# Optimization experiments

Hardware: AMD Instinct MI355X
Metric: run time of the kernel (lower is better)

The kernel has to match this reference:

```python
import jax, jax.numpy as jnp
import numpy as np

H = 512

def _gru_layer(x, W_ih, W_hh, b_ih, b_hh):
    # x: [T, B, D_in]; PyTorch gate order: r, z, n
    xg = jnp.einsum('tbd,gd->tbg', x, W_ih) + b_ih  # [T, B, 3H], input projections for all steps
    h0 = jnp.zeros((x.shape[1], W_hh.shape[1]), x.dtype)

    def step(h, xg_t):
        hg = h @ W_hh.T + b_hh                      # [B, 3H]
        xr, xz, xn = jnp.split(xg_t, 3, axis=-1)
        hr, hz, hn = jnp.split(hg, 3, axis=-1)
        r = jax.nn.sigmoid(xr + hr)
        z = jax.nn.sigmoid(xz + hz)
        n = jnp.tanh(xn + r * hn)
        h_new = (1.0 - z) * n + z * h
        return h_new, h_new

    hT, ys = jax.lax.scan(step, h0, xg)
    return ys, hT  # [T, B, H], [B, H]


def setup_inputs() -> dict:
    key = jax.random.key(0)
    ks = jax.random.split(key, 10)
    D, T, B, L = 256, 512, 64, 2
    s = 1.0 / np.sqrt(H)  # PyTorch uniform(-1/sqrt(H), 1/sqrt(H)) init
    u = lambda k, shape: jax.random.uniform(k, shape, jnp.float32, -s, s)
    return {
        'x': jax.random.normal(ks[0], (T, B, D), jnp.float32),
        'W_ih0': u(ks[1], (3 * H, D)),
        'W_hh0': u(ks[2], (3 * H, H)),
        'b_ih0': u(ks[3], (3 * H,)),
        'b_hh0': u(ks[4], (3 * H,)),
        'W_ih1': u(ks[5], (3 * H, H)),
        'W_hh1': u(ks[6], (3 * H, H)),
        'b_ih1': u(ks[7], (3 * H,)),
        'b_hh1': u(ks[8], (3 * H,)),
    }


def reference(x, W_ih0, W_hh0, b_ih0, b_hh0, W_ih1, W_hh1, b_ih1, b_hh1):
    y0, h0 = _gru_layer(x, W_ih0, W_hh0, b_ih0, b_hh0)
    y1, h1 = _gru_layer(y0, W_ih1, W_hh1, b_ih1, b_hh1)
    hn = jnp.stack([h0, h1], axis=0)  # [num_layers, B, H]
    return (y1, hn)
```

## Files before the change

kernel.cpp:

```cpp
#include <hip/hip_runtime.h>
#include <math.h>

#define Hh   512
#define G3   1536
#define Tlen 512
#define Bsz  64
#define BH   (Bsz*Hh)

__device__ __forceinline__ float sigmoid_f(float x) { return 1.0f / (1.0f + expf(-x)); }

__device__ __forceinline__ void store_coh(float* p, float v) {
  asm volatile("global_store_dword %0, %1, off sc0 sc1" :: "v"(p), "v"(v) : "memory");
}

__global__ __launch_bounds__(256) void gemm_xg(const float* __restrict__ A,
                                               const float* __restrict__ W,
                                               const float* __restrict__ bias,
                                               float* __restrict__ C,
                                               int M, int N, int K) {
  __shared__ float As[16][132];
  __shared__ float Bs[16][132];
  const int nbm = M >> 7;
  const int bm = blockIdx.x % nbm;
  const int bn = blockIdx.x / nbm;
  const int m0 = bm << 7, n0 = bn << 7;
  const int tid = threadIdx.x;
  const int tx = tid & 15, ty = tid >> 4;

  const int row0 = tid >> 2;
  const int kq0  = (tid & 3) << 2;

  const float* Ap0 = &A[(size_t)(m0 + row0) * K + kq0];
  const float* Ap1 = &A[(size_t)(m0 + row0 + 64) * K + kq0];
  const float* Wp0 = &W[(size_t)(n0 + row0) * K + kq0];
  const float* Wp1 = &W[(size_t)(n0 + row0 + 64) * K + kq0];

  float4 ra0 = *(const float4*)(Ap0);
  float4 ra1 = *(const float4*)(Ap1);
  float4 rb0 = *(const float4*)(Wp0);
  float4 rb1 = *(const float4*)(Wp1);

  float acc[8][8];
#pragma unroll
  for (int r = 0; r < 8; r++)
#pragma unroll
    for (int c = 0; c < 8; c++) acc[r][c] = 0.0f;

  for (int kk = 0; kk < K; kk += 16) {
    As[kq0+0][row0]    = ra0.x; As[kq0+1][row0]    = ra0.y; As[kq0+2][row0]    = ra0.z; As[kq0+3][row0]    = ra0.w;
    As[kq0+0][row0+64] = ra1.x; As[kq0+1][row0+64] = ra1.y; As[kq0+2][row0+64] = ra1.z; As[kq0+3][row0+64] = ra1.w;
    Bs[kq0+0][row0]    = rb0.x; Bs[kq0+1][row0]    = rb0.y; Bs[kq0+2][row0]    = rb0.z; Bs[kq0+3][row0]    = rb0.w;
    Bs[kq0+0][row0+64] = rb1.x; Bs[kq0+1][row0+64] = rb1.y; Bs[kq0+2][row0+64] = rb1.z; Bs[kq0+3][row0+64] = rb1.w;
    __syncthreads();
    const int kn = kk + 16;
    if (kn < K) {
      ra0 = *(const float4*)(Ap0 + kn);
      ra1 = *(const float4*)(Ap1 + kn);
      rb0 = *(const float4*)(Wp0 + kn);
      rb1 = *(const float4*)(Wp1 + kn);
    }
#pragma unroll
    for (int k = 0; k < 16; k++) {
      float4 a0 = *(const float4*)&As[k][ty << 3];
      float4 a1 = *(const float4*)&As[k][(ty << 3) + 4];
      float4 b0 = *(const float4*)&Bs[k][tx << 3];
      float4 b1 = *(const float4*)&Bs[k][(tx << 3) + 4];
      float ar[8] = {a0.x, a0.y, a0.z, a0.w, a1.x, a1.y, a1.z, a1.w};
      float br[8] = {b0.x, b0.y, b0.z, b0.w, b1.x, b1.y, b1.z, b1.w};
#pragma unroll
      for (int r = 0; r < 8; r++)
#pragma unroll
        for (int c = 0; c < 8; c++) acc[r][c] = fmaf(ar[r], br[c], acc[r][c]);
    }
    __syncthreads();
  }
  float bl[8];
#pragma unroll
  for (int c = 0; c < 8; c++) bl[c] = bias[n0 + (tx << 3) + c];
#pragma unroll
  for (int r = 0; r < 8; r++) {
    int m = m0 + (ty << 3) + r;
    float4 o0 = make_float4(acc[r][0] + bl[0], acc[r][1] + bl[1], acc[r][2] + bl[2], acc[r][3] + bl[3]);
    float4 o1 = make_float4(acc[r][4] + bl[4], acc[r][5] + bl[5], acc[r][6] + bl[6], acc[r][7] + bl[7]);
    *(float4*)&C[(size_t)m * N + n0 + (tx << 3)]     = o0;
    *(float4*)&C[(size_t)m * N + n0 + (tx << 3) + 4] = o1;
  }
}

__global__ __launch_bounds__(256, 1) void gru_scan(
    const float* __restrict__ xg,
    const float* __restrict__ Whh,
    const float* __restrict__ bhh,
    float* __restrict__ y,
    float* __restrict__ hfin,
    float* hbuf,
    int* slots,
    int base) {
  const int tid = threadIdx.x;
  const int jl = tid >> 4;
  const int ks = tid & 15;
  const int bgrp = blockIdx.x & 7;
  const int jgrp = blockIdx.x >> 3;
  const int j0 = jgrp << 4;
  const int b0 = bgrp << 3;
  const int k0 = ks << 5;

  int* myslot = slots + (bgrp * 32 + jgrp) * 32;
  int* gslots = slots + bgrp * 32 * 32;

  __shared__ float4 hs4[8 * 128];

  float4 wv[3][8];
#pragma unroll
  for (int g = 0; g < 3; g++) {
    const float* wp = &Whh[(size_t)(g * Hh + j0 + jl) * Hh + k0];
#pragma unroll
    for (int q = 0; q < 8; q++) wv[g][q] = *(const float4*)&wp[q * 4];
  }
  float bh[3];
#pragma unroll
  for (int g = 0; g < 3; g++) bh[g] = bhh[g * Hh + j0 + jl];

  int off[8];
#pragma unroll
  for (int q = 0; q < 8; q++) off[q] = (ks * 8 + q) ^ (ks & 7);

  const int fq = tid & 127;
  const int brow = tid >> 7;
  const int fswz = fq ^ ((fq >> 3) & 7);

  float xr = 0.0f, xz = 0.0f, xn = 0.0f;
  if (ks < 8) {
    const float* xp = &xg[(size_t)(b0 + ks) * G3 + j0 + jl];
    xr = xp[0]; xz = xp[Hh]; xn = xp[2 * Hh];
  }

  int cur = 0;

  for (int t = 0; t < Tlen; t++) {
    const float4* hsrc = (const float4*)(hbuf + cur * BH) + (size_t)(b0 + brow) * 128 + fq;
    float4 h0, h1, h2, h3;
    {
      const float4* p0 = hsrc;
      const float4* p1 = hsrc + 2 * 128;
      const float4* p2 = hsrc + 4 * 128;
      const float4* p3 = hsrc + 6 * 128;
      asm volatile(
          "global_load_dwordx4 %0, %4, off sc0 sc1\n\t"
          "global_load_dwordx4 %1, %5, off sc0 sc1\n\t"
          "global_load_dwordx4 %2, %6, off sc0 sc1\n\t"
          "global_load_dwordx4 %3, %7, off sc0 sc1\n\t"
          "s_waitcnt vmcnt(0)"
          : "=&v"(h0), "=&v"(h1), "=&v"(h2), "=&v"(h3)
          : "v"(p0), "v"(p1), "v"(p2), "v"(p3)
          : "memory");
    }
    hs4[(brow + 0) * 128 + fswz] = h0;
    hs4[(brow + 2) * 128 + fswz] = h1;
    hs4[(brow + 4) * 128 + fswz] = h2;
    hs4[(brow + 6) * 128 + fswz] = h3;
    __syncthreads();

    float acc[3][8];
#pragma unroll
    for (int b = 0; b < 8; b++) {
      float4 hv[8];
#pragma unroll
      for (int q = 0; q < 8; q++) hv[q] = hs4[b * 128 + off[q]];
#pragma unroll
      for (int g = 0; g < 3; g++) {
        float s = 0.0f;
#pragma unroll
        for (int q = 0; q < 8; q++) {
          s = fmaf(wv[g][q].x, hv[q].x, s);
          s = fmaf(wv[g][q].y, hv[q].y, s);
          s = fmaf(wv[g][q].z, hv[q].z, s);
          s = fmaf(wv[g][q].w, hv[q].w, s);
        }
        acc[g][b] = s;
      }
    }
#pragma unroll
    for (int d = 1; d < 16; d <<= 1) {
#pragma unroll
      for (int g = 0; g < 3; g++)
#pragma unroll
        for (int b = 0; b < 8; b++) acc[g][b] += __shfl_xor(acc[g][b], d);
    }

    if (ks < 8) {
      int b = b0 + ks;
      int e = j0 + jl;
      float r = sigmoid_f(xr + acc[0][ks] + bh[0]);
      float z = sigmoid_f(xz + acc[1][ks] + bh[1]);
      float n = tanhf(xn + r * (acc[2][ks] + bh[2]));
      int f = e >> 2;
      float4 hp4 = hs4[ks * 128 + (f ^ ((f >> 3) & 7))];
      float hp = ((const float*)&hp4)[e & 3];
      float hnew = (1.0f - z) * n + z * hp;
      store_coh(&hbuf[(cur ^ 1) * BH + (size_t)b * Hh + e], hnew);
      y[((size_t)t * Bsz + b) * Hh + e] = hnew;
      if (t == Tlen - 1) hfin[(size_t)b * Hh + e] = hnew;
    }

    if (t == Tlen - 1) break;

    __syncthreads();

    if (tid == 0) {
      __hip_atomic_store(myslot, base + t + 1, __ATOMIC_RELAXED, __HIP_MEMORY_SCOPE_AGENT);
    }

    float nxr = 0.0f, nxz = 0.0f, nxn = 0.0f;
    if (ks < 8) {
      const float* xp = &xg[((size_t)(t + 1) * Bsz + (b0 + ks)) * G3 + j0 + jl];
      nxr = xp[0]; nxz = xp[Hh]; nxn = xp[2 * Hh];
    }

    if (tid < 64) {
      const int target = base + t + 1;
      for (;;) {
        int v = (tid < 32)
            ? __hip_atomic_load(gslots + tid * 32, __ATOMIC_RELAXED, __HIP_MEMORY_SCOPE_AGENT)
            : 0x7FFFFFFF;
        if (!__any(v < target)) break;
        __builtin_amdgcn_s_sleep(1);
      }
    }
    __syncthreads();

    xr = nxr; xz = nxz; xn = nxn;
    cur ^= 1;
  }
}

extern "C" void kernel_launch(void* const* d_in, const int* in_sizes, int n_in,
                              void* d_out, int out_size, void* d_ws, size_t ws_size,
                              hipStream_t stream) {
  const float* x     = (const float*)d_in[0];
  const float* Wih0  = (const float*)d_in[1];
  const float* Whh0  = (const float*)d_in[2];
  const float* bih0  = (const float*)d_in[3];
  const float* bhh0  = (const float*)d_in[4];
  const float* Wih1  = (const float*)d_in[5];
  const float* Whh1  = (const float*)d_in[6];
  const float* bih1  = (const float*)d_in[7];
  const float* bhh1  = (const float*)d_in[8];

  float* out = (float*)d_out;
  float* y1   = out;
  float* hn0  = out + (size_t)Tlen * BH;
  float* hn1  = hn0 + BH;

  float* ws    = (float*)d_ws;
  int*   slots = (int*)d_ws;
  float* hbuf  = ws + 8192;
  float* xgbuf = hbuf + 4 * BH;
  float* y0    = xgbuf + (size_t)Tlen * Bsz * G3;

  const int M = Tlen * Bsz;

  hipMemsetAsync(slots, 0, 8 * 32 * 32 * sizeof(int), stream);
  hipMemsetAsync(hbuf, 0, BH * sizeof(float), stream);
  hipMemsetAsync(hbuf + 2 * BH, 0, BH * sizeof(float), stream);

  dim3 gemm_grid((M / 128) * (G3 / 128));

  gemm_xg<<<gemm_grid, 256, 0, stream>>>(x, Wih0, bih0, xgbuf, M, G3, 256);
  gru_scan<<<256, 256, 0, stream>>>(xgbuf, Whh0, bhh0, y0, hn0, hbuf, slots, 0);

  gemm_xg<<<gemm_grid, 256, 0, stream>>>(y0, Wih1, bih1, xgbuf, M, G3, 512);
  gru_scan<<<256, 256, 0, stream>>>(xgbuf, Whh1, bhh1, y1, hn1, hbuf + 2 * BH, slots, Tlen);
}
```

Baseline: 5.867 ms.

## Fuse both GRU layers into one wavefront-pipelined persistent kernel

Replaces the two sequential scan kernels and the second input-projection GEMM with a single persistent kernel of 512 blocks. Half the blocks run layer 0 and the other half run layer 1, which computes its input projection per step from y0 using register-resident Wih1. Layer 1 waits on per-step flags from layer 0 and from its own blocks, so the two recurrences overlap in a wavefront instead of running back to back. The cost is double the register weight footprint for layer-1 blocks and a launch-bounds occupancy of 2 blocks per CU. It also adds cross-layer spin-wait traffic and relies on all 512 blocks being co-resident to avoid deadlock.

```diff
diff --git a/kernel.cpp b/kernel.cpp
--- a/kernel.cpp
+++ b/kernel.cpp
@@ -87,150 +87,304 @@
   }
 }
 
-__global__ __launch_bounds__(256, 1) void gru_scan(
-    const float* __restrict__ xg,
-    const float* __restrict__ Whh,
-    const float* __restrict__ bhh,
-    float* __restrict__ y,
-    float* __restrict__ hfin,
-    float* hbuf,
-    int* slots,
-    int base) {
+__global__ __launch_bounds__(256, 2) void gru_fused(
+    const float* __restrict__ xg0,
+    const float* __restrict__ Whh0,
+    const float* __restrict__ bhh0,
+    const float* __restrict__ Wih1,
+    const float* __restrict__ bih1,
+    const float* __restrict__ Whh1,
+    const float* __restrict__ bhh1,
+    float* __restrict__ y1,
+    float* __restrict__ hn0,
+    float* __restrict__ hn1,
+    float* h0buf, float* h1buf,
+    float* y0buf,
+    int* l0slots, int* l1slots) {
   const int tid = threadIdx.x;
   const int jl = tid >> 4;
   const int ks = tid & 15;
   const int bgrp = blockIdx.x & 7;
-  const int jgrp = blockIdx.x >> 3;
+  const int rr   = blockIdx.x >> 3;
+  const int role = rr & 1;
+  const int jgrp = rr >> 1;
   const int j0 = jgrp << 4;
   const int b0 = bgrp << 3;
   const int k0 = ks << 5;
 
-  int* myslot = slots + (bgrp * 32 + jgrp) * 32;
-  int* gslots = slots + bgrp * 32 * 32;
-
-  __shared__ float4 hs4[8 * 128];
-
-  float4 wv[3][8];
-#pragma unroll
-  for (int g = 0; g < 3; g++) {
-    const float* wp = &Whh[(size_t)(g * Hh + j0 + jl) * Hh + k0];
-#pragma unroll
-    for (int q = 0; q < 8; q++) wv[g][q] = *(const float4*)&wp[q * 4];
-  }
-  float bh[3];
-#pragma unroll
-  for (int g = 0; g < 3; g++) bh[g] = bhh[g * Hh + j0 + jl];
+  __shared__ float4 hs4[2][1024];
+
+  int* myl0 = l0slots + (bgrp * 32 + jgrp) * 32;
+  int* gl0  = l0slots + bgrp * 32 * 32;
+  int* myl1 = l1slots + (bgrp * 32 + jgrp) * 32;
+  int* gl1  = l1slots + bgrp * 32 * 32;
 
   int off[8];
 #pragma unroll
   for (int q = 0; q < 8; q++) off[q] = (ks * 8 + q) ^ (ks & 7);
-
   const int fq = tid & 127;
   const int brow = tid >> 7;
   const int fswz = fq ^ ((fq >> 3) & 7);
 
-  float xr = 0.0f, xz = 0.0f, xn = 0.0f;
-  if (ks < 8) {
-    const float* xp = &xg[(size_t)(b0 + ks) * G3 + j0 + jl];
-    xr = xp[0]; xz = xp[Hh]; xn = xp[2 * Hh];
-  }
-
-  int cur = 0;
-
-  for (int t = 0; t < Tlen; t++) {
-    const float4* hsrc = (const float4*)(hbuf + cur * BH) + (size_t)(b0 + brow) * 128 + fq;
-    float4 h0, h1, h2, h3;
-    {
-      const float4* p0 = hsrc;
-      const float4* p1 = hsrc + 2 * 128;
-      const float4* p2 = hsrc + 4 * 128;
-      const float4* p3 = hsrc + 6 * 128;
-      asm volatile(
-          "global_load_dwordx4 %0, %4, off sc0 sc1\n\t"
-          "global_load_dwordx4 %1, %5, off sc0 sc1\n\t"
-          "global_load_dwordx4 %2, %6, off sc0 sc1\n\t"
-          "global_load_dwordx4 %3, %7, off sc0 sc1\n\t"
-          "s_waitcnt vmcnt(0)"
-          : "=&v"(h0), "=&v"(h1), "=&v"(h2), "=&v"(h3)
-          : "v"(p0), "v"(p1), "v"(p2), "v"(p3)
-          : "memory");
-    }
-    hs4[(brow + 0) * 128 + fswz] = h0;
-    hs4[(brow + 2) * 128 + fswz] = h1;
-    hs4[(brow + 4) * 128 + fswz] = h2;
-    hs4[(brow + 6) * 128 + fswz] = h3;
-    __syncthreads();
-
-    float acc[3][8];
-#pragma unroll
-    for (int b = 0; b < 8; b++) {
-      float4 hv[8];
-#pragma unroll
-      for (int q = 0; q < 8; q++) hv[q] = hs4[b * 128 + off[q]];
-#pragma unroll
-      for (int g = 0; g < 3; g++) {
-        float s = 0.0f;
-#pragma unroll
-        for (int q = 0; q < 8; q++) {
-          s = fmaf(wv[g][q].x, hv[q].x, s);
-          s = fmaf(wv[g][q].y, hv[q].y, s);
-          s = fmaf(wv[g][q].z, hv[q].z, s);
-          s = fmaf(wv[g][q].w, hv[q].w, s);
+  if (role == 0) {
+    float4 wv[3][8];
+#pragma unroll
+    for (int g = 0; g < 3; g++) {
+      const float* wp = &Whh0[(size_t)(g * Hh + j0 + jl) * Hh + k0];
+#pragma unroll
+      for (int q = 0; q < 8; q++) wv[g][q] = *(const float4*)&wp[q * 4];
+    }
+    float bh[3];
+#pragma unroll
+    for (int g = 0; g < 3; g++) bh[g] = bhh0[g * Hh + j0 + jl];
+
+    float xr = 0.0f, xz = 0.0f, xn = 0.0f;
+    if (ks < 8) {
+      const float* xp = &xg0[(size_t)(b0 + ks) * G3 + j0 + jl];
+      xr = xp[0]; xz = xp[Hh]; xn = xp[2 * Hh];
+    }
+
+    int cur = 0;
+    for (int t = 0; t < Tlen; t++) {
+      const float4* hsrc = (const float4*)(h0buf + cur * BH) + (size_t)(b0 + brow) * 128 + fq;
+      float4 h0, h1, h2, h3;
+      {
+        const float4* p0 = hsrc;
+        const float4* p1 = hsrc + 2 * 128;
+        const float4* p2 = hsrc + 4 * 128;
+        const float4* p3 = hsrc + 6 * 128;
+        asm volatile(
+            "global_load_dwordx4 %0, %4, off sc0 sc1\n\t"
+            "global_load_dwordx4 %1, %5, off sc0 sc1\n\t"
+            "global_load_dwordx4 %2, %6, off sc0 sc1\n\t"
+            "global_load_dwordx4 %3, %7, off sc0 sc1\n\t"
+            "s_waitcnt vmcnt(0)"
+            : "=&v"(h0), "=&v"(h1), "=&v"(h2), "=&v"(h3)
+            : "v"(p0), "v"(p1), "v"(p2), "v"(p3)
+            : "memory");
+      }
+      hs4[0][(brow + 0) * 128 + fswz] = h0;
+      hs4[0][(brow + 2) * 128 + fswz] = h1;
+      hs4[0][(brow + 4) * 128 + fswz] = h2;
+      hs4[0][(brow + 6) * 128 + fswz] = h3;
+      __syncthreads();
+
+      float acc[3][8];
+#pragma unroll
+      for (int b = 0; b < 8; b++) {
+        float4 hv[8];
+#pragma unroll
+        for (int q = 0; q < 8; q++) hv[q] = hs4[0][b * 128 + off[q]];
+#pragma unroll
+        for (int g = 0; g < 3; g++) {
+          float s = 0.0f;
+#pragma unroll
+          for (int q = 0; q < 8; q++) {
+            s = fmaf(wv[g][q].x, hv[q].x, s);
+            s = fmaf(wv[g][q].y, hv[q].y, s);
+            s = fmaf(wv[g][q].z, hv[q].z, s);
+            s = fmaf(wv[g][q].w, hv[q].w, s);
+          }
+          acc[g][b] = s;
         }
-        acc[g][b] = s;
-      }
-    }
-#pragma unroll
-    for (int d = 1; d < 16; d <<= 1) {
-#pragma unroll
-      for (int g = 0; g < 3; g++)
-#pragma unroll
-        for (int b = 0; b < 8; b++) acc[g][b] += __shfl_xor(acc[g][b], d);
-    }
-
-    if (ks < 8) {
-      int b = b0 + ks;
-      int e = j0 + jl;
-      float r = sigmoid_f(xr + acc[0][ks] + bh[0]);
-      float z = sigmoid_f(xz + acc[1][ks] + bh[1]);
-      float n = tanhf(xn + r * (acc[2][ks] + bh[2]));
-      int f = e >> 2;
-      float4 hp4 = hs4[ks * 128 + (f ^ ((f >> 3) & 7))];
-      float hp = ((const float*)&hp4)[e & 3];
-      float hnew = (1.0f - z) * n + z * hp;
-      store_coh(&hbuf[(cur ^ 1) * BH + (size_t)b * Hh + e], hnew);
-      y[((size_t)t * Bsz + b) * Hh + e] = hnew;
-      if (t == Tlen - 1) hfin[(size_t)b * Hh + e] = hnew;
-    }
-
-    if (t == Tlen - 1) break;
-
-    __syncthreads();
-
-    if (tid == 0) {
-      __hip_atomic_store(myslot, base + t + 1, __ATOMIC_RELAXED, __HIP_MEMORY_SCOPE_AGENT);
-    }
-
-    float nxr = 0.0f, nxz = 0.0f, nxn = 0.0f;
-    if (ks < 8) {
-      const float* xp = &xg[((size_t)(t + 1) * Bsz + (b0 + ks)) * G3 + j0 + jl];
-      nxr = xp[0]; nxz = xp[Hh]; nxn = xp[2 * Hh];
-    }
-
-    if (tid < 64) {
-      const int target = base + t + 1;
-      for (;;) {
-        int v = (tid < 32)
-            ? __hip_atomic_load(gslots + tid * 32, __ATOMIC_RELAXED, __HIP_MEMORY_SCOPE_AGENT)
-            : 0x7FFFFFFF;
-        if (!__any(v < target)) break;
-        __builtin_amdgcn_s_sleep(1);
-      }
-    }
-    __syncthreads();
-
-    xr = nxr; xz = nxz; xn = nxn;
-    cur ^= 1;
+      }
+#pragma unroll
+      for (int d = 1; d < 16; d <<= 1) {
+#pragma unroll
+        for (int g = 0; g < 3; g++)
+#pragma unroll
+          for (int b = 0; b < 8; b++) acc[g][b] += __shfl_xor(acc[g][b], d);
+      }
+
+      if (ks < 8) {
+        int b = b0 + ks;
+        int e = j0 + jl;
+        float r = sigmoid_f(xr + acc[0][ks] + bh[0]);
+        float z = sigmoid_f(xz + acc[1][ks] + bh[1]);
+        float n = tanhf(xn + r * (acc[2][ks] + bh[2]));
+        int f = e >> 2;
+        float4 hp4 = hs4[0][ks * 128 + (f ^ ((f >> 3) & 7))];
+        float hp = ((const float*)&hp4)[e & 3];
+        float hnew = (1.0f - z) * n + z * hp;
+        store_coh(&h0buf[(cur ^ 1) * BH + (size_t)b * Hh + e], hnew);
+        store_coh(&y0buf[((size_t)t * Bsz + b) * Hh + e], hnew);
+        if (t == Tlen - 1) hn0[(size_t)b * Hh + e] = hnew;
+      }
+
+      __syncthreads();
+      if (tid == 0) {
+        __hip_atomic_store(myl0, t + 1, __ATOMIC_RELAXED, __HIP_MEMORY_SCOPE_AGENT);
+      }
+      if (t == Tlen - 1) break;
+
+      float nxr = 0.0f, nxz = 0.0f, nxn = 0.0f;
+      if (ks < 8) {
+        const float* xp = &xg0[((size_t)(t + 1) * Bsz + (b0 + ks)) * G3 + j0 + jl];
+        nxr = xp[0]; nxz = xp[Hh]; nxn = xp[2 * Hh];
+      }
+      if (tid < 64) {
+        const int target = t + 1;
+        for (;;) {
+          int v = (tid < 32)
+              ? __hip_atomic_load(gl0 + tid * 32, __ATOMIC_RELAXED, __HIP_MEMORY_SCOPE_AGENT)
+              : 0x7FFFFFFF;
+          if (!__any(v < target)) break;
+          __builtin_amdgcn_s_sleep(1);
+        }
+      }
+      __syncthreads();
+      xr = nxr; xz = nxz; xn = nxn;
+      cur ^= 1;
+    }
+  } else {
+    float4 wi[3][8], wh[3][8];
+#pragma unroll
+    for (int g = 0; g < 3; g++) {
+      const float* wip = &Wih1[(size_t)(g * Hh + j0 + jl) * Hh + k0];
+      const float* whp = &Whh1[(size_t)(g * Hh + j0 + jl) * Hh + k0];
+#pragma unroll
+      for (int q = 0; q < 8; q++) {
+        wi[g][q] = *(const float4*)&wip[q * 4];
+        wh[g][q] = *(const float4*)&whp[q * 4];
+      }
+    }
+    float bi[3], bh[3];
+#pragma unroll
+    for (int g = 0; g < 3; g++) {
+      bi[g] = bih1[g * Hh + j0 + jl];
+      bh[g] = bhh1[g * Hh + j0 + jl];
+    }
+
+    int cur = 0;
+    for (int t = 0; t < Tlen; t++) {
+      if (tid < 64) {
+        const int target = t + 1;
+        for (;;) {
+          int v;
+          if (tid < 32)
+            v = __hip_atomic_load(gl0 + tid * 32, __ATOMIC_RELAXED, __HIP_MEMORY_SCOPE_AGENT);
+          else
+            v = __hip_atomic_load(gl1 + (tid - 32) * 32, __ATOMIC_RELAXED, __HIP_MEMORY_SCOPE_AGENT) + 1;
+          if (!__any(v < target)) break;
+          __builtin_amdgcn_s_sleep(1);
+        }
+      }
+      __syncthreads();
+
+      const float4* ysrc = (const float4*)(y0buf + (size_t)t * BH) + (size_t)(b0 + brow) * 128 + fq;
+      const float4* hsrc = (const float4*)(h1buf + cur * BH) + (size_t)(b0 + brow) * 128 + fq;
+      float4 a0, a1, a2, a3, c0, c1, c2, c3;
+      {
+        const float4* p0 = ysrc;
+        const float4* p1 = ysrc + 2 * 128;
+        const float4* p2 = ysrc + 4 * 128;
+        const float4* p3 = ysrc + 6 * 128;
+        const float4* q0 = hsrc;
+        const float4* q1 = hsrc + 2 * 128;
+        const float4* q2 = hsrc + 4 * 128;
+        const float4* q3 = hsrc + 6 * 128;
+        asm volatile(
+            "global_load_dwordx4 %0, %8, off sc0 sc1\n\t"
+            "global_load_dwordx4 %1, %9, off sc0 sc1\n\t"
+            "global_load_dwordx4 %2, %10, off sc0 sc1\n\t"
+            "global_load_dwordx4 %3, %11, off sc0 sc1\n\t"
+            "global_load_dwordx4 %4, %12, off sc0 sc1\n\t"
+            "global_load_dwordx4 %5, %13, off sc0 sc1\n\t"
+            "global_load_dwordx4 %6, %14, off sc0 sc1\n\t"
+            "global_load_dwordx4 %7, %15, off sc0 sc1\n\t"
+            "s_waitcnt vmcnt(0)"
+            : "=&v"(a0), "=&v"(a1), "=&v"(a2), "=&v"(a3),
+              "=&v"(c0), "=&v"(c1), "=&v"(c2), "=&v"(c3)
+            : "v"(p0), "v"(p1), "v"(p2), "v"(p3),
+              "v"(q0), "v"(q1), "v"(q2), "v"(q3)
+            : "memory");
+      }
+      hs4[0][(brow + 0) * 128 + fswz] = a0;
+      hs4[0][(brow + 2) * 128 + fswz] = a1;
+      hs4[0][(brow + 4) * 128 + fswz] = a2;
+      hs4[0][(brow + 6) * 128 + fswz] = a3;
+      hs4[1][(brow + 0) * 128 + fswz] = c0;
+      hs4[1][(brow + 2) * 128 + fswz] = c1;
+      hs4[1][(brow + 4) * 128 + fswz] = c2;
+      hs4[1][(brow + 6) * 128 + fswz] = c3;
+      __syncthreads();
+
+      float xga[3][8];
+#pragma unroll
+      for (int b = 0; b < 8; b++) {
+        float4 hv[8];
+#pragma unroll
+        for (int q = 0; q < 8; q++) hv[q] = hs4[0][b * 128 + off[q]];
+#pragma unroll
+        for (int g = 0; g < 3; g++) {
+          float s = 0.0f;
+#pragma unroll
+          for (int q = 0; q < 8; q++) {
+            s = fmaf(wi[g][q].x, hv[q].x, s);
+            s = fmaf(wi[g][q].y, hv[q].y, s);
+            s = fmaf(wi[g][q].z, hv[q].z, s);
+            s = fmaf(wi[g][q].w, hv[q].w, s);
+          }
+          xga[g][b] = s;
+        }
+      }
+#pragma unroll
+      for (int d = 1; d < 16; d <<= 1) {
+#pragma unroll
+        for (int g = 0; g < 3; g++)
+#pragma unroll
+          for (int b = 0; b < 8; b++) xga[g][b] += __shfl_xor(xga[g][b], d);
+      }
+
+      float acc[3][8];
+#pragma unroll
+      for (int b = 0; b < 8; b++) {
+        float4 hv[8];
+#pragma unroll
+        for (int q = 0; q < 8; q++) hv[q] = hs4[1][b * 128 + off[q]];
+#pragma unroll
+        for (int g = 0; g < 3; g++) {
+          float s = 0.0f;
+#pragma unroll
+          for (int q = 0; q < 8; q++) {
+            s = fmaf(wh[g][q].x, hv[q].x, s);
+            s = fmaf(wh[g][q].y, hv[q].y, s);
+            s = fmaf(wh[g][q].z, hv[q].z, s);
+            s = fmaf(wh[g][q].w, hv[q].w, s);
+          }
+          acc[g][b] = s;
+        }
+      }
+#pragma unroll
+      for (int d = 1; d < 16; d <<= 1) {
+#pragma unroll
+        for (int g = 0; g < 3; g++)
+#pragma unroll
+          for (int b = 0; b < 8; b++) acc[g][b] += __shfl_xor(acc[g][b], d);
+      }
+
+      if (ks < 8) {
+        int b = b0 + ks;
+        int e = j0 + jl;
+        float r = sigmoid_f(xga[0][ks] + bi[0] + acc[0][ks] + bh[0]);
+        float z = sigmoid_f(xga[1][ks] + bi[1] + acc[1][ks] + bh[1]);
+        float n = tanhf(xga[2][ks] + bi[2] + r * (acc[2][ks] + bh[2]));
+        int f = e >> 2;
+        float4 hp4 = hs4[1][ks * 128 + (f ^ ((f >> 3) & 7))];
+        float hp = ((const float*)&hp4)[e & 3];
+        float hnew = (1.0f - z) * n + z * hp;
+        store_coh(&h1buf[(cur ^ 1) * BH + (size_t)b * Hh + e], hnew);
+        y1[((size_t)t * Bsz + b) * Hh + e] = hnew;
+        if (t == Tlen - 1) hn1[(size_t)b * Hh + e] = hnew;
+      }
+
+      if (t == Tlen - 1) break;
+      __syncthreads();
+      if (tid == 0) {
+        __hip_atomic_store(myl1, t + 1, __ATOMIC_RELAXED, __HIP_MEMORY_SCOPE_AGENT);
+      }
+      cur ^= 1;
+    }
   }
 }
 
@@ -252,23 +406,25 @@
   float* hn0  = out + (size_t)Tlen * BH;
   float* hn1  = hn0 + BH;
 
-  float* ws    = (float*)d_ws;
-  int*   slots = (int*)d_ws;
-  float* hbuf  = ws + 8192;
-  float* xgbuf = hbuf + 4 * BH;
-  float* y0    = xgbuf + (size_t)Tlen * Bsz * G3;
+  float* ws     = (float*)d_ws;
+  int*   l0slots = (int*)d_ws;
+  int*   l1slots = l0slots + 8192;
+  float* h0buf  = ws + 16384;
+  float* h1buf  = h0buf + 2 * BH;
+  float* xg0buf = h1buf + 2 * BH;
+  float* y0buf  = xg0buf + (size_t)Tlen * Bsz * G3;
 
   const int M = Tlen * Bsz;
 
-  hipMemsetAsync(slots, 0, 8 * 32 * 32 * sizeof(int), stream);
-  hipMemsetAsync(hbuf, 0, BH * sizeof(float), stream);
-  hipMemsetAsync(hbuf + 2 * BH, 0, BH * sizeof(float), stream);
+  hipMemsetAsync(l0slots, 0, 2 * 8192 * sizeof(int), stream);
+  hipMemsetAsync(h0buf, 0, BH * sizeof(float), stream);
+  hipMemsetAsync(h1buf, 0, BH * sizeof(float), stream);
 
   dim3 gemm_grid((M / 128) * (G3 / 128));
 
-  gemm_xg<<<gemm_grid, 256, 0, stream>>>(x, Wih0, bih0, xgbuf, M, G3, 256);
-  gru_scan<<<256, 256, 0, stream>>>(xgbuf, Whh0, bhh0, y0, hn0, hbuf, slots, 0);
-
-  gemm_xg<<<gemm_grid, 256, 0, stream>>>(y0, Wih1, bih1, xgbuf, M, G3, 512);
-  gru_scan<<<256, 256, 0, stream>>>(xgbuf, Whh1, bhh1, y1, hn1, hbuf + 2 * BH, slots, Tlen);
+  gemm_xg<<<gemm_grid, 256, 0, stream>>>(x, Wih0, bih0, xg0buf, M, G3, 256);
+
+  gru_fused<<<512, 256, 0, stream>>>(xg0buf, Whh0, bhh0, Wih1, bih1, Whh1, bhh1,
+                                     y1, hn0, hn1, h0buf, h1buf, y0buf,
+                                     l0slots, l1slots);
 }
```

Result: slower. 20.32 ms (+246.3%).

## Replace block barriers with per-wavefront flags in GRU scan grid sync

Applied to the files above, without the earlier changes.

The per-step __syncthreads plus single-thread flag publish is replaced by per-wavefront flags: each wave waits for its own stores, publishes its own slot, and every wave polls all 128 wave slots of its batch group itself. The y store is also moved after the flag publish so it stays off the critical path. This removes two block-wide barriers per timestep from the recurrence. In exchange there are four times as many slots to poll and more polling traffic. Safety now depends on per-wave vmcnt ordering and on the next step's shared-memory h reload needing no block barrier, which is not visible here.

```diff
diff --git a/kernel.cpp b/kernel.cpp
--- a/kernel.cpp
+++ b/kernel.cpp
@@ -105,8 +105,8 @@
   const int b0 = bgrp << 3;
   const int k0 = ks << 5;
 
-  int* myslot = slots + (bgrp * 32 + jgrp) * 32;
-  int* gslots = slots + bgrp * 32 * 32;
+  int* gslots  = slots + bgrp * 1024;
+  int* blkslot = gslots + jgrp * 32;
 
   __shared__ float4 hs4[8 * 128];
 
@@ -188,46 +188,52 @@
         for (int b = 0; b < 8; b++) acc[g][b] += __shfl_xor(acc[g][b], d);
     }
 
+    float hnew = 0.0f;
+    int b = 0, e = 0;
     if (ks < 8) {
-      int b = b0 + ks;
-      int e = j0 + jl;
+      b = b0 + ks;
+      e = j0 + jl;
       float r = sigmoid_f(xr + acc[0][ks] + bh[0]);
       float z = sigmoid_f(xz + acc[1][ks] + bh[1]);
       float n = tanhf(xn + r * (acc[2][ks] + bh[2]));
       int f = e >> 2;
       float4 hp4 = hs4[ks * 128 + (f ^ ((f >> 3) & 7))];
       float hp = ((const float*)&hp4)[e & 3];
-      float hnew = (1.0f - z) * n + z * hp;
+      hnew = (1.0f - z) * n + z * hp;
       store_coh(&hbuf[(cur ^ 1) * BH + (size_t)b * Hh + e], hnew);
-      y[((size_t)t * Bsz + b) * Hh + e] = hnew;
-      if (t == Tlen - 1) hfin[(size_t)b * Hh + e] = hnew;
-    }
-
-    if (t == Tlen - 1) break;
-
-    __syncthreads();
-
-    if (tid == 0) {
-      __hip_atomic_store(myslot, base + t + 1, __ATOMIC_RELAXED, __HIP_MEMORY_SCOPE_AGENT);
-    }
-
+    }
+
+    if (t == Tlen - 1) {
+      if (ks < 8) {
+        y[((size_t)t * Bsz + b) * Hh + e] = hnew;
+        hfin[(size_t)b * Hh + e] = hnew;
+      }
+      break;
+    }
+
+    asm volatile("s_waitcnt vmcnt(0)" ::: "memory");
+    if ((tid & 63) == 0) {
+      __hip_atomic_store(blkslot + (tid >> 6) * 8, base + t + 1,
+                         __ATOMIC_RELAXED, __HIP_MEMORY_SCOPE_AGENT);
+    }
+
+    if (ks < 8) y[((size_t)t * Bsz + b) * Hh + e] = hnew;
     float nxr = 0.0f, nxz = 0.0f, nxn = 0.0f;
     if (ks < 8) {
       const float* xp = &xg[((size_t)(t + 1) * Bsz + (b0 + ks)) * G3 + j0 + jl];
       nxr = xp[0]; nxz = xp[Hh]; nxn = xp[2 * Hh];
     }
 
-    if (tid < 64) {
+    {
+      const int lane = tid & 63;
       const int target = base + t + 1;
       for (;;) {
-        int v = (tid < 32)
-            ? __hip_atomic_load(gslots + tid * 32, __ATOMIC_RELAXED, __HIP_MEMORY_SCOPE_AGENT)
-            : 0x7FFFFFFF;
-        if (!__any(v < target)) break;
+        int v0 = __hip_atomic_load(gslots + lane * 8, __ATOMIC_RELAXED, __HIP_MEMORY_SCOPE_AGENT);
+        int v1 = __hip_atomic_load(gslots + (lane + 64) * 8, __ATOMIC_RELAXED, __HIP_MEMORY_SCOPE_AGENT);
+        if (!__any((v0 < target) || (v1 < target))) break;
         __builtin_amdgcn_s_sleep(1);
       }
     }
-    __syncthreads();
 
     xr = nxr; xz = nxz; xn = nxn;
     cur ^= 1;
@@ -260,7 +266,7 @@
 
   const int M = Tlen * Bsz;
 
-  hipMemsetAsync(slots, 0, 8 * 32 * 32 * sizeof(int), stream);
+  hipMemsetAsync(slots, 0, 8192 * sizeof(int), stream);
   hipMemsetAsync(hbuf, 0, BH * sizeof(float), stream);
   hipMemsetAsync(hbuf + 2 * BH, 0, BH * sizeof(float), stream);
 
```

After: 8.065 ms. 37.5% more time.
